# Kernel tuning notes

Measured on AMD Instinct MI355X. Metric: run time of the kernel, lower is better.

Reference implementation:

```python
import jax, jax.numpy as jnp
import numpy as np

VOCAB, EMB, HID, B, T = 50000, 16, 32, 4096, 500


def setup_inputs() -> dict:
    key = jax.random.key(0)
    k1, k2, k3, k4 = jax.random.split(key, 4)
    tokens = jax.random.randint(k1, (B, T), 0, VOCAB, dtype=jnp.int32)
    emb_table = jax.random.normal(k2, (VOCAB, EMB), dtype=jnp.float32) * 0.05
    kernel = jax.random.normal(k3, (EMB, 4 * HID), dtype=jnp.float32) * (1.0 / np.sqrt(EMB))
    rec_kernel = jax.random.normal(k4, (HID, 4 * HID), dtype=jnp.float32) * (1.0 / np.sqrt(HID))
    # Keras default: unit_forget_bias=True -> forget-gate bias = 1
    bias = jnp.concatenate([
        jnp.zeros((HID,), jnp.float32),
        jnp.ones((HID,), jnp.float32),
        jnp.zeros((2 * HID,), jnp.float32),
    ])
    return {"tokens": tokens, "emb_table": emb_table, "kernel": kernel,
            "rec_kernel": rec_kernel, "bias": bias}


def reference(tokens, emb_table, kernel, rec_kernel, bias):
    # Embedding with mask_zero=True: mask = tokens != 0
    embedded = emb_table[tokens]                 # [B, T, EMB]
    mask = (tokens != 0)                         # [B, T] bool
    # Precompute input projections for all timesteps (one big GEMM)
    x_proj = jnp.einsum('bte,eh->bth', embedded, kernel) + bias  # [B, T, 4H]

    def step(carry, xs):
        h, c = carry                              # [B, H] each
        xp_t, m_t = xs                            # [B, 4H], [B]
        z = xp_t + h @ rec_kernel                 # [B, 4H]
        i, f, g, o = jnp.split(z, 4, axis=-1)     # Keras gate order i,f,c,o
        i = jax.nn.sigmoid(i)
        f = jax.nn.sigmoid(f)
        g = jnp.tanh(g)
        o = jax.nn.sigmoid(o)
        c_new = f * c + i * g
        h_new = o * jnp.tanh(c_new)
        m = m_t[:, None]
        # masked steps carry previous state through (Keras LSTM mask semantics)
        h = jnp.where(m, h_new, h)
        c = jnp.where(m, c_new, c)
        return (h, c), None

    h0 = jnp.zeros((tokens.shape[0], HID), jnp.float32)
    c0 = jnp.zeros((tokens.shape[0], HID), jnp.float32)
    xs = (jnp.swapaxes(x_proj, 0, 1), jnp.swapaxes(mask, 0, 1))  # time-major
    (h, c), _ = jax.lax.scan(step, (h0, c0), xs)
    return h                                      # [B, HID] last (masked) output
```

## Files before the change

### kernel.cpp

```cpp
#include <hip/hip_runtime.h>
#include <cstdint>

#define VOCAB_N 50000
#define EMB_N   16
#define HID_N   32
#define B_N     4096
#define T_N     500
#define TPAD    512

__device__ __forceinline__ float frcp(float x) { return __builtin_amdgcn_rcpf(x); }

__global__ void build_proj2_kernel(const float* __restrict__ emb,
                                   const float* __restrict__ W,
                                   const float* __restrict__ bias,
                                   float2* __restrict__ proj2) {
  __shared__ float Wl[EMB_N * 128];
  __shared__ float bl[128];
  const int tid = threadIdx.x;
  for (int i = tid; i < EMB_N * 128 / 4; i += 256)
    reinterpret_cast<float4*>(Wl)[i] = reinterpret_cast<const float4*>(W)[i];
  if (tid < 32)
    reinterpret_cast<float4*>(bl)[tid] = reinterpret_cast<const float4*>(bias)[tid];
  __syncthreads();

  const int gid = blockIdx.x * 256 + tid;
  const int v = gid >> 6;
  const int l = gid & 63;
  if (v >= VOCAB_N) return;

  const float4* ev = reinterpret_cast<const float4*>(emb + (size_t)v * EMB_N);
  float4 e0 = ev[0], e1 = ev[1], e2 = ev[2], e3 = ev[3];
  const float em[16] = {e0.x,e0.y,e0.z,e0.w, e1.x,e1.y,e1.z,e1.w,
                        e2.x,e2.y,e2.z,e2.w, e3.x,e3.y,e3.z,e3.w};
  float a0 = bl[l], a1 = bl[64 + l];
#pragma unroll
  for (int e = 0; e < EMB_N; ++e) {
    a0 = fmaf(em[e], Wl[e * 128 + l],      a0);
    a1 = fmaf(em[e], Wl[e * 128 + 64 + l], a1);
  }
  proj2[(size_t)v * 64 + l] = make_float2(a0, a1);
}

#define LSTM_STEP(STOK, PTOK, PCUR)                                           \
  {                                                                           \
    const float xA = (PCUR).x, xB = (PCUR).y;                                 \
    (PCUR) = proj2[(size_t)(PTOK) * 64 + l];                \
    float a0 = xA, a1 = xB, b0 = 0.f, b1 = 0.f;                               \
    _Pragma("unroll")                                                         \
    for (int q = 0; q < 8; ++q) {                                             \
      const float4 hq = h4[q];                                                \
      a0 = fmaf(hq.x, wr0[4*q+0], a0); a1 = fmaf(hq.x, wr1[4*q+0], a1);       \
      b0 = fmaf(hq.y, wr0[4*q+1], b0); b1 = fmaf(hq.y, wr1[4*q+1], b1);       \
      a0 = fmaf(hq.z, wr0[4*q+2], a0); a1 = fmaf(hq.z, wr1[4*q+2], a1);       \
      b0 = fmaf(hq.w, wr0[4*q+3], b0); b1 = fmaf(hq.w, wr1[4*q+3], b1);       \
    }                                                                         \
    const float zA = a0 + b0;                                                 \
    const float zB = a1 + b1;                                                 \
    if ((STOK) != 0) {                                                        \
      float eA = exp2f(zA * -1.4426950408889634f);                            \
      float P  = frcp(1.0f + eA);                                             \
      float eB = exp2f(zB * sB);                                              \
      float rB = frcp(1.0f + eB);                                             \
      float Q  = fmaf(mB, rB, aB);                                            \
      float P2 = __shfl_xor(P, 32);                                           \
      float Q2 = __shfl_xor(Q, 32);                                           \
      float gi = lo ? P  : P2;                                                \
      float gf = lo ? P2 : P;                                                 \
      float gg = lo ? Q  : Q2;                                                \
      float go = lo ? Q2 : Q;                                                 \
      float cn = fmaf(gf, c, gi * gg);                                        \
      float eC = exp2f(cn * 2.8853900817779268f);                             \
      float tc = fmaf(-2.0f, frcp(1.0f + eC), 1.0f);                          \
      float hn = go * tc;                                                     \
      c = cn; h = hn;                                                         \
      hrow[kidx] = hn;                                                        \
      _Pragma("unroll")                                                       \
      for (int q = 0; q < 8; ++q)                                             \
        h4[q] = reinterpret_cast<const float4*>(hrow)[q];                     \
    }                                                                         \
  }

__global__ __launch_bounds__(256, 3)
void lstm_scan3_kernel(const int*    __restrict__ tokens,
                       const float*  __restrict__ rec_kernel,
                       const float2* __restrict__ proj2,
                       float*        __restrict__ out) {
  __shared__ int   tokl[4][TPAD];
  __shared__ float hbuf[4][HID_N];

  const int tid  = threadIdx.x;
  const int wrow = tid >> 6;
  const int lane = tid & 63;
  const int l    = lane;
  const int row  = blockIdx.x * 4 + wrow;

  {
    const int4* src = reinterpret_cast<const int4*>(tokens + (size_t)blockIdx.x * 4 * T_N);
    for (int i = tid; i < 4 * T_N / 4; i += 256) {
      int4 v4 = src[i];
      int g = 4 * i;
      int r = g / T_N;
      int cidx = g - r * T_N;
      *reinterpret_cast<int4*>(&tokl[r][cidx]) = v4;
    }
    if (tid < 48) {
      int r = tid / 12, cc = T_N + (tid % 12);
      tokl[r][cc] = 0;
    }
  }

  float wr0[HID_N], wr1[HID_N];
#pragma unroll
  for (int k = 0; k < HID_N; ++k) {
    wr0[k] = rec_kernel[k * 128 + l];
    wr1[k] = rec_kernel[k * 128 + 64 + l];
  }

  const bool lo = (lane < 32);
  const float sB = lo ?  2.8853900817779268f : -1.4426950408889634f;
  const float mB = lo ? -2.0f : 1.0f;
  const float aB = lo ?  1.0f : 0.0f;

  __syncthreads();

  float c = 0.0f, h = 0.0f;
  float4 h4[8];
#pragma unroll
  for (int q = 0; q < 8; ++q) h4[q] = make_float4(0.f, 0.f, 0.f, 0.f);

  float* hrow = &hbuf[wrow][0];
  const int kidx = lane & 31;

  int t0 = __builtin_amdgcn_readfirstlane(tokl[wrow][0]);
  int t1 = __builtin_amdgcn_readfirstlane(tokl[wrow][1]);
  int t2 = __builtin_amdgcn_readfirstlane(tokl[wrow][2]);
  int t3 = __builtin_amdgcn_readfirstlane(tokl[wrow][3]);

  float2 p0 = proj2[(size_t)t0 * 64 + l];
  float2 p1 = proj2[(size_t)t1 * 64 + l];

#pragma unroll 1
  for (int t = 0; t < T_N; t += 2) {
    int2 tv = *reinterpret_cast<const int2*>(&tokl[wrow][t + 4]);

    LSTM_STEP(t0, t2, p0);
    LSTM_STEP(t1, t3, p1);

    t0 = t2; t1 = t3;
    t2 = __builtin_amdgcn_readfirstlane(tv.x);
    t3 = __builtin_amdgcn_readfirstlane(tv.y);
  }

  if (lane < 32) out[(size_t)row * HID_N + lane] = h;
}

__device__ __forceinline__ float sigm_fb(float x) {
  return frcp(1.0f + exp2f(x * -1.4426950408889634f));
}
__device__ __forceinline__ float tanh_fb(float x) {
  float e = exp2f(x * 2.8853900817779268f);
  return fmaf(-2.0f, frcp(e + 1.0f), 1.0f);
}

__global__ __launch_bounds__(256, 2)
void lstm_scan_fallback(const int*   __restrict__ tokens,
                        const float* __restrict__ rec_kernel,
                        const float* __restrict__ emb,
                        const float* __restrict__ W,
                        const float* __restrict__ bias,
                        float*       __restrict__ out) {
  __shared__ int   tokl[8][T_N];
  __shared__ float hbuf[8][HID_N];

  const int tid  = threadIdx.x;
  const int wv   = tid >> 6;
  const int lane = tid & 63;
  const int half = lane >> 5;
  const int j    = lane & 31;
  const int wrow = wv * 2 + half;
  const int row  = blockIdx.x * 8 + wrow;

  {
    const int4* src = reinterpret_cast<const int4*>(tokens + (size_t)blockIdx.x * 8 * T_N);
    int4* dst = reinterpret_cast<int4*>(&tokl[0][0]);
    for (int i = tid; i < 8 * T_N / 4; i += 256) dst[i] = src[i];
  }

  float wr[HID_N][4];
#pragma unroll
  for (int k = 0; k < HID_N; ++k)
#pragma unroll
    for (int g = 0; g < 4; ++g) wr[k][g] = rec_kernel[k * 128 + g * 32 + j];

  float wk[EMB_N][4];
  float bb[4];
#pragma unroll
  for (int e = 0; e < EMB_N; ++e)
#pragma unroll
    for (int g = 0; g < 4; ++g) wk[e][g] = W[e * 128 + g * 32 + j];
#pragma unroll
  for (int g = 0; g < 4; ++g) bb[g] = bias[g * 32 + j];
  __syncthreads();

  float c = 0.0f, h = 0.0f;
  float4 h4[8];
#pragma unroll
  for (int q = 0; q < 8; ++q) h4[q] = make_float4(0.f, 0.f, 0.f, 0.f);

  for (int t = 0; t < T_N; ++t) {
    const int tokc = tokl[wrow][t];
    const float4* ev = reinterpret_cast<const float4*>(emb + (size_t)tokc * EMB_N);
    float4 e0 = ev[0], e1 = ev[1], e2 = ev[2], e3 = ev[3];
    const float em[16] = {e0.x,e0.y,e0.z,e0.w, e1.x,e1.y,e1.z,e1.w,
                          e2.x,e2.y,e2.z,e2.w, e3.x,e3.y,e3.z,e3.w};
    float a0 = bb[0], a1 = bb[1], a2 = bb[2], a3 = bb[3];
#pragma unroll
    for (int e = 0; e < EMB_N; ++e) {
      float x = em[e];
      a0 = fmaf(x, wk[e][0], a0); a1 = fmaf(x, wk[e][1], a1);
      a2 = fmaf(x, wk[e][2], a2); a3 = fmaf(x, wk[e][3], a3);
    }
#pragma unroll
    for (int q = 0; q < 8; ++q) {
      float hx = h4[q].x, hy = h4[q].y, hz = h4[q].z, hw = h4[q].w;
      a0 = fmaf(hx, wr[4*q+0][0], a0); a1 = fmaf(hx, wr[4*q+0][1], a1);
      a2 = fmaf(hx, wr[4*q+0][2], a2); a3 = fmaf(hx, wr[4*q+0][3], a3);
      a0 = fmaf(hy, wr[4*q+1][0], a0); a1 = fmaf(hy, wr[4*q+1][1], a1);
      a2 = fmaf(hy, wr[4*q+1][2], a2); a3 = fmaf(hy, wr[4*q+1][3], a3);
      a0 = fmaf(hz, wr[4*q+2][0], a0); a1 = fmaf(hz, wr[4*q+2][1], a1);
      a2 = fmaf(hz, wr[4*q+2][2], a2); a3 = fmaf(hz, wr[4*q+2][3], a3);
      a0 = fmaf(hw, wr[4*q+3][0], a0); a1 = fmaf(hw, wr[4*q+3][1], a1);
      a2 = fmaf(hw, wr[4*q+3][2], a2); a3 = fmaf(hw, wr[4*q+3][3], a3);
    }
    float ig = sigm_fb(a0), fg = sigm_fb(a1), gg = tanh_fb(a2), og = sigm_fb(a3);
    float cn = fmaf(fg, c, ig * gg);
    float hn = og * tanh_fb(cn);
    if (tokc != 0) { h = hn; c = cn; }
    hbuf[wrow][j] = h;
    asm volatile("" ::: "memory");
#pragma unroll
    for (int q = 0; q < 8; ++q)
      h4[q] = reinterpret_cast<const float4*>(&hbuf[wrow][0])[q];
    asm volatile("" ::: "memory");
  }
  out[(size_t)row * HID_N + j] = h;
}

extern "C" void kernel_launch(void* const* d_in, const int* in_sizes, int n_in,
                              void* d_out, int out_size, void* d_ws, size_t ws_size,
                              hipStream_t stream) {
  const int*   tokens = (const int*)  d_in[0];
  const float* emb    = (const float*)d_in[1];
  const float* W      = (const float*)d_in[2];
  const float* rec    = (const float*)d_in[3];
  const float* bias   = (const float*)d_in[4];
  float* out = (float*)d_out;

  const size_t need = (size_t)VOCAB_N * 64 * sizeof(float2);
  if (ws_size >= need) {
    float2* proj2 = (float2*)d_ws;
    build_proj2_kernel<<<(VOCAB_N * 64) / 256 + 1, 256, 0, stream>>>(emb, W, bias, proj2);
    lstm_scan3_kernel<<<B_N / 4, 256, 0, stream>>>(tokens, rec, proj2, out);
  } else {
    lstm_scan_fallback<<<B_N / 8, 256, 0, stream>>>(tokens, rec, emb, W, bias, out);
  }
}
```

Measured before the change: 399.8 us.

## Use packed FP32 FMA for recurrent matvec with one wave per block

Rewrites the recurrent LSTM kernel to run one 64-lane wave per block (one batch row) instead of four waves per block. The h-times-recurrent-weight dot product now uses two-wide packed FMAs over paired weights, and h is reloaded from LDS at the start of each step instead of being copied into registers after the write. A compiler memory barrier replaces the block-wide sync. The intent is to halve FMA issue count on the serial critical path and drop cross-wave block structure, at the risk of relying on implicit wave-level LDS ordering and using more, smaller blocks.

```diff
diff --git a/kernel.cpp b/kernel.cpp
--- a/kernel.cpp
+++ b/kernel.cpp
@@ -6,9 +6,11 @@
 #define HID_N   32
 #define B_N     4096
 #define T_N     500
-#define TPAD    512
+
+typedef __attribute__((ext_vector_type(2))) float f32x2;
 
 __device__ __forceinline__ float frcp(float x) { return __builtin_amdgcn_rcpf(x); }
+#define FMA2(A, B, C) __builtin_elementwise_fma((A), (B), (C))
 
 __global__ void build_proj2_kernel(const float* __restrict__ emb,
                                    const float* __restrict__ W,
@@ -41,22 +43,35 @@
   proj2[(size_t)v * 64 + l] = make_float2(a0, a1);
 }
 
-#define LSTM_STEP(STOK, PTOK, PCUR)                                           \
+#define KP(HX, HY, K2, AA, BB)                                                \
+    (AA) = FMA2(((f32x2){(HX), (HY)}), wA[K2], (AA));                         \
+    (BB) = FMA2(((f32x2){(HX), (HY)}), wB[K2], (BB));
+
+#define STEP(STOK, PTOK, PC)                                                  \
   {                                                                           \
-    const float xA = (PCUR).x, xB = (PCUR).y;                                 \
-    (PCUR) = proj2[(size_t)(PTOK) * 64 + l];                \
-    float a0 = xA, a1 = xB, b0 = 0.f, b1 = 0.f;                               \
-    _Pragma("unroll")                                                         \
-    for (int q = 0; q < 8; ++q) {                                             \
-      const float4 hq = h4[q];                                                \
-      a0 = fmaf(hq.x, wr0[4*q+0], a0); a1 = fmaf(hq.x, wr1[4*q+0], a1);       \
-      b0 = fmaf(hq.y, wr0[4*q+1], b0); b1 = fmaf(hq.y, wr1[4*q+1], b1);       \
-      a0 = fmaf(hq.z, wr0[4*q+2], a0); a1 = fmaf(hq.z, wr1[4*q+2], a1);       \
-      b0 = fmaf(hq.w, wr0[4*q+3], b0); b1 = fmaf(hq.w, wr1[4*q+3], b1);       \
-    }                                                                         \
-    const float zA = a0 + b0;                                                 \
-    const float zB = a1 + b1;                                                 \
-    if ((STOK) != 0) {                                                        \
+    float4 hq0 = *reinterpret_cast<const float4*>(hbuf + 0);                  \
+    float4 hq1 = *reinterpret_cast<const float4*>(hbuf + 4);                  \
+    float4 hq2 = *reinterpret_cast<const float4*>(hbuf + 8);                  \
+    float4 hq3 = *reinterpret_cast<const float4*>(hbuf + 12);                 \
+    float4 hq4 = *reinterpret_cast<const float4*>(hbuf + 16);                 \
+    float4 hq5 = *reinterpret_cast<const float4*>(hbuf + 20);                 \
+    float4 hq6 = *reinterpret_cast<const float4*>(hbuf + 24);                 \
+    float4 hq7 = *reinterpret_cast<const float4*>(hbuf + 28);                 \
+    const float xA = (PC).x, xB = (PC).y;                                     \
+    (PC) = proj2[(size_t)(PTOK) * 64 + l];                  \
+    f32x2 a0 = {xA, 0.f}, a1 = {0.f, 0.f};                                    \
+    f32x2 b0 = {xB, 0.f}, b1 = {0.f, 0.f};                                    \
+    KP(hq0.x, hq0.y,  0, a0, b0)  KP(hq0.z, hq0.w,  1, a0, b0)                \
+    KP(hq1.x, hq1.y,  2, a0, b0)  KP(hq1.z, hq1.w,  3, a0, b0)                \
+    KP(hq2.x, hq2.y,  4, a0, b0)  KP(hq2.z, hq2.w,  5, a0, b0)                \
+    KP(hq3.x, hq3.y,  6, a0, b0)  KP(hq3.z, hq3.w,  7, a0, b0)                \
+    KP(hq4.x, hq4.y,  8, a1, b1)  KP(hq4.z, hq4.w,  9, a1, b1)                \
+    KP(hq5.x, hq5.y, 10, a1, b1)  KP(hq5.z, hq5.w, 11, a1, b1)                \
+    KP(hq6.x, hq6.y, 12, a1, b1)  KP(hq6.z, hq6.w, 13, a1, b1)                \
+    KP(hq7.x, hq7.y, 14, a1, b1)  KP(hq7.z, hq7.w, 15, a1, b1)                \
+    const float zA = (a0.x + a1.x) + (a0.y + a1.y);                           \
+    const float zB = (b0.x + b1.x) + (b0.y + b1.y);                           \
+    if ((STOK) != 0) {                               \
       float eA = exp2f(zA * -1.4426950408889634f);                            \
       float P  = frcp(1.0f + eA);                                             \
       float eB = exp2f(zB * sB);                                              \
@@ -73,85 +88,69 @@
       float tc = fmaf(-2.0f, frcp(1.0f + eC), 1.0f);                          \
       float hn = go * tc;                                                     \
       c = cn; h = hn;                                                         \
-      hrow[kidx] = hn;                                                        \
-      _Pragma("unroll")                                                       \
-      for (int q = 0; q < 8; ++q)                                             \
-        h4[q] = reinterpret_cast<const float4*>(hrow)[q];                     \
+      hbuf[kidx] = hn;                                                        \
+      asm volatile("" ::: "memory");                                          \
     }                                                                         \
   }
 
-__global__ __launch_bounds__(256, 3)
-void lstm_scan3_kernel(const int*    __restrict__ tokens,
-                       const float*  __restrict__ rec_kernel,
-                       const float2* __restrict__ proj2,
-                       float*        __restrict__ out) {
-  __shared__ int   tokl[4][TPAD];
-  __shared__ float hbuf[4][HID_N];
-
-  const int tid  = threadIdx.x;
-  const int wrow = tid >> 6;
-  const int lane = tid & 63;
-  const int l    = lane;
-  const int row  = blockIdx.x * 4 + wrow;
+__global__ __launch_bounds__(64, 4)
+void lstm_pk_kernel(const int*    __restrict__ tokens,
+                    const float*  __restrict__ rec_kernel,
+                    const float2* __restrict__ proj2,
+                    float*        __restrict__ out) {
+  __shared__ int   tokl[520];
+  __shared__ float hbuf[32];
+
+  const int l   = threadIdx.x;
+  const int row = blockIdx.x;
+  const int kidx = l & 31;
 
   {
-    const int4* src = reinterpret_cast<const int4*>(tokens + (size_t)blockIdx.x * 4 * T_N);
-    for (int i = tid; i < 4 * T_N / 4; i += 256) {
-      int4 v4 = src[i];
-      int g = 4 * i;
-      int r = g / T_N;
-      int cidx = g - r * T_N;
-      *reinterpret_cast<int4*>(&tokl[r][cidx]) = v4;
-    }
-    if (tid < 48) {
-      int r = tid / 12, cc = T_N + (tid % 12);
-      tokl[r][cc] = 0;
-    }
-  }
-
-  float wr0[HID_N], wr1[HID_N];
-#pragma unroll
-  for (int k = 0; k < HID_N; ++k) {
-    wr0[k] = rec_kernel[k * 128 + l];
-    wr1[k] = rec_kernel[k * 128 + 64 + l];
-  }
-
-  const bool lo = (lane < 32);
+    const int4* src = reinterpret_cast<const int4*>(tokens + (size_t)row * T_N);
+    for (int i = l; i < T_N / 4; i += 64)
+      *reinterpret_cast<int4*>(&tokl[4 * i]) = src[i];
+    if (l < 20) tokl[T_N + l] = 0;
+  }
+  if (l < 32) hbuf[l] = 0.0f;
+  asm volatile("" ::: "memory");
+
+  f32x2 wA[16], wB[16];
+#pragma unroll
+  for (int k2 = 0; k2 < 16; ++k2) {
+    wA[k2] = (f32x2){ rec_kernel[(2 * k2) * 128 + l],
+                      rec_kernel[(2 * k2 + 1) * 128 + l] };
+    wB[k2] = (f32x2){ rec_kernel[(2 * k2) * 128 + 64 + l],
+                      rec_kernel[(2 * k2 + 1) * 128 + 64 + l] };
+  }
+
+  const bool lo = (l < 32);
   const float sB = lo ?  2.8853900817779268f : -1.4426950408889634f;
   const float mB = lo ? -2.0f : 1.0f;
   const float aB = lo ?  1.0f : 0.0f;
 
-  __syncthreads();
-
   float c = 0.0f, h = 0.0f;
-  float4 h4[8];
-#pragma unroll
-  for (int q = 0; q < 8; ++q) h4[q] = make_float4(0.f, 0.f, 0.f, 0.f);
-
-  float* hrow = &hbuf[wrow][0];
-  const int kidx = lane & 31;
-
-  int t0 = __builtin_amdgcn_readfirstlane(tokl[wrow][0]);
-  int t1 = __builtin_amdgcn_readfirstlane(tokl[wrow][1]);
-  int t2 = __builtin_amdgcn_readfirstlane(tokl[wrow][2]);
-  int t3 = __builtin_amdgcn_readfirstlane(tokl[wrow][3]);
+
+  int t0 = __builtin_amdgcn_readfirstlane(tokl[0]);
+  int t1 = __builtin_amdgcn_readfirstlane(tokl[1]);
+  int t2 = __builtin_amdgcn_readfirstlane(tokl[2]);
+  int t3 = __builtin_amdgcn_readfirstlane(tokl[3]);
 
   float2 p0 = proj2[(size_t)t0 * 64 + l];
   float2 p1 = proj2[(size_t)t1 * 64 + l];
 
 #pragma unroll 1
   for (int t = 0; t < T_N; t += 2) {
-    int2 tv = *reinterpret_cast<const int2*>(&tokl[wrow][t + 4]);
-
-    LSTM_STEP(t0, t2, p0);
-    LSTM_STEP(t1, t3, p1);
+    int2 tv = *reinterpret_cast<const int2*>(&tokl[t + 4]);
+
+    STEP(t0, t2, p0);
+    STEP(t1, t3, p1);
 
     t0 = t2; t1 = t3;
     t2 = __builtin_amdgcn_readfirstlane(tv.x);
     t3 = __builtin_amdgcn_readfirstlane(tv.y);
   }
 
-  if (lane < 32) out[(size_t)row * HID_N + lane] = h;
+  if (l < 32) out[(size_t)row * HID_N + l] = h;
 }
 
 __device__ __forceinline__ float sigm_fb(float x) {
@@ -190,16 +189,16 @@
 #pragma unroll
   for (int k = 0; k < HID_N; ++k)
 #pragma unroll
-    for (int g = 0; g < 4; ++g) wr[k][g] = rec_kernel[k * 128 + g * 32 + j];
+    for (int gg2 = 0; gg2 < 4; ++gg2) wr[k][gg2] = rec_kernel[k * 128 + gg2 * 32 + j];
 
   float wk[EMB_N][4];
   float bb[4];
 #pragma unroll
   for (int e = 0; e < EMB_N; ++e)
 #pragma unroll
-    for (int g = 0; g < 4; ++g) wk[e][g] = W[e * 128 + g * 32 + j];
-#pragma unroll
-  for (int g = 0; g < 4; ++g) bb[g] = bias[g * 32 + j];
+    for (int gg2 = 0; gg2 < 4; ++gg2) wk[e][gg2] = W[e * 128 + gg2 * 32 + j];
+#pragma unroll
+  for (int gg2 = 0; gg2 < 4; ++gg2) bb[gg2] = bias[gg2 * 32 + j];
   __syncthreads();
 
   float c = 0.0f, h = 0.0f;
@@ -260,7 +259,7 @@
   if (ws_size >= need) {
     float2* proj2 = (float2*)d_ws;
     build_proj2_kernel<<<(VOCAB_N * 64) / 256 + 1, 256, 0, stream>>>(emb, W, bias, proj2);
-    lstm_scan3_kernel<<<B_N / 4, 256, 0, stream>>>(tokens, rec, proj2, out);
+    lstm_pk_kernel<<<B_N, 64, 0, stream>>>(tokens, rec, proj2, out);
   } else {
     lstm_scan_fallback<<<B_N / 8, 256, 0, stream>>>(tokens, rec, emb, W, bias, out);
   }
```

Measured after the change: 389.1 us. -2.7%, faster.
